# Optimization experiments

Measured on AMD Instinct MI355X. Metric: run time of the kernel, lower is better.

Reference implementation:

```python
import jax, jax.numpy as jnp
import numpy as np

HEADS = 8
DIM_HEAD = 64
QUERY_DIM = 512
CONTEXT_DIM = 768
INNER = HEADS * DIM_HEAD  # 512
SCALE = DIM_HEAD ** -0.5


def setup_inputs() -> dict:
    key = jax.random.key(0)
    ks = jax.random.split(key, 7)
    B, N, M = 4, 2048, 2048
    x = jax.random.normal(ks[0], (B, N, QUERY_DIM), dtype=jnp.float32)
    context = jax.random.normal(ks[1], (B, M, CONTEXT_DIM), dtype=jnp.float32)
    # torch Linear weights: [out_features, in_features], y = x @ W.T
    s = 0.02
    Wq = jax.random.normal(ks[2], (INNER, QUERY_DIM), dtype=jnp.float32) * s
    Wk = jax.random.normal(ks[3], (INNER, CONTEXT_DIM), dtype=jnp.float32) * s
    Wv = jax.random.normal(ks[4], (INNER, CONTEXT_DIM), dtype=jnp.float32) * s
    Wo = jax.random.normal(ks[5], (QUERY_DIM, INNER), dtype=jnp.float32) * s
    bo = jax.random.normal(ks[6], (QUERY_DIM,), dtype=jnp.float32) * s
    return {"x": x, "context": context, "Wq": Wq, "Wk": Wk, "Wv": Wv, "Wo": Wo, "bo": bo}


def reference(x, context, Wq, Wk, Wv, Wo, bo):
    b, n, _ = x.shape
    m = context.shape[1]
    h, d = HEADS, DIM_HEAD
    # Projections (bias=False for q/k/v)
    q = jnp.einsum('bnc,ec->bne', x, Wq)        # [b, n, inner]
    k = jnp.einsum('bmc,ec->bme', context, Wk)  # [b, m, inner]
    v = jnp.einsum('bmc,ec->bme', context, Wv)
    # Split heads
    q = q.reshape(b, n, h, d)
    k = k.reshape(b, m, h, d)
    v = v.reshape(b, m, h, d)
    # Scores in fp32 (original casts q,k to float), scaled by dim_head**-0.5
    sim = jnp.einsum('bihd,bjhd->bhij', q.astype(jnp.float32), k.astype(jnp.float32)) * SCALE
    attn = jax.nn.softmax(sim, axis=-1).astype(v.dtype)
    out = jnp.einsum('bhij,bjhd->bihd', attn, v).reshape(b, n, h * d)
    # Output projection with bias (dropout=0 -> identity)
    return jnp.einsum('bne,oe->bno', out, Wo) + bo
```

## Files before the change

### kernel.cpp

```cpp
#include <hip/hip_runtime.h>
#include <hip/hip_bf16.h>
#include <math.h>


typedef __bf16 bf16x8 __attribute__((ext_vector_type(8)));
typedef __bf16 bf16x4 __attribute__((ext_vector_type(4)));
typedef float f32x4 __attribute__((ext_vector_type(4)));

#define QSCALE 0.18033688011112042f

#if __has_builtin(__builtin_amdgcn_exp2f)
#define EXP2(x) __builtin_amdgcn_exp2f(x)
#else
#define EXP2(x) exp2f(x)
#endif

__device__ __forceinline__ f32x4 mfma32(bf16x8 a, bf16x8 b, f32x4 c) {
  return __builtin_amdgcn_mfma_f32_16x16x32_bf16(a, b, c, 0, 0, 0);
}

__device__ __forceinline__ void st_cast16(__bf16* dst, float4 f0, float4 f1,
                                          float4 f2, float4 f3) {
  union { __bf16 b[16]; uint4 u[2]; } cv;
  cv.b[0] = (__bf16)f0.x;  cv.b[1] = (__bf16)f0.y;
  cv.b[2] = (__bf16)f0.z;  cv.b[3] = (__bf16)f0.w;
  cv.b[4] = (__bf16)f1.x;  cv.b[5] = (__bf16)f1.y;
  cv.b[6] = (__bf16)f1.z;  cv.b[7] = (__bf16)f1.w;
  cv.b[8] = (__bf16)f2.x;  cv.b[9] = (__bf16)f2.y;
  cv.b[10] = (__bf16)f2.z; cv.b[11] = (__bf16)f2.w;
  cv.b[12] = (__bf16)f3.x; cv.b[13] = (__bf16)f3.y;
  cv.b[14] = (__bf16)f3.z; cv.b[15] = (__bf16)f3.w;
  ((uint4*)dst)[0] = cv.u[0];
  ((uint4*)dst)[1] = cv.u[1];
}

__global__ __launch_bounds__(256) void cast_w(
    const float* __restrict__ wq, const float* __restrict__ wk,
    const float* __restrict__ wv, const float* __restrict__ wo,
    __bf16* __restrict__ wqb, __bf16* __restrict__ wkb,
    __bf16* __restrict__ wvb, __bf16* __restrict__ wob) {
  const int B0 = 65536;
  const int B1 = 163840;
  const int B2 = 262144;
  const int B3 = 327680;
  for (int i = blockIdx.x * blockDim.x + threadIdx.x; i < B3;
       i += gridDim.x * blockDim.x) {
    const float* s;
    __bf16* d;
    int off;
    if (i < B0)      { s = wq; d = wqb; off = i; }
    else if (i < B1) { s = wk; d = wkb; off = i - B0; }
    else if (i < B2) { s = wv; d = wvb; off = i - B1; }
    else             { s = wo; d = wob; off = i - B2; }
    float4 f = ((const float4*)s)[off];
    union { __bf16 b[4]; ushort4 u; } cv;
    cv.b[0] = (__bf16)f.x; cv.b[1] = (__bf16)f.y;
    cv.b[2] = (__bf16)f.z; cv.b[3] = (__bf16)f.w;
    ((ushort4*)d)[off] = cv.u;
  }
}

template <int MODE>
__device__ __forceinline__ void gemm_body(
    const float* __restrict__ A, const __bf16* __restrict__ W,
    __bf16* __restrict__ Cout, int Kd, float scale, int m0, int n0,
    __bf16 (*As)[72], __bf16 (*Bs)[72]) {
  const int t = threadIdx.x;
  const int w = t >> 6;
  const int lane = t & 63;
  const int ln = lane & 15;
  const int qd = lane >> 4;
  const int wm = (w >> 1) * 64;
  const int wn = (w & 1) * 64;

  f32x4 zero4 = {0.f, 0.f, 0.f, 0.f};
  f32x4 acc[4][4];
#pragma unroll
  for (int i = 0; i < 4; ++i)
#pragma unroll
    for (int j = 0; j < 4; ++j) acc[i][j] = zero4;

  const int r0 = t >> 2;
  const int c0 = (t & 3) * 16;
  const float* gA0 = A + (size_t)(m0 + r0) * Kd + c0;
  const float* gA1 = A + (size_t)(m0 + r0 + 64) * Kd + c0;
  const __bf16* gB0 = W + (size_t)(n0 + r0) * Kd + c0;
  const __bf16* gB1 = W + (size_t)(n0 + r0 + 64) * Kd + c0;

  float4 a0[4], a1[4];
#pragma unroll
  for (int j = 0; j < 4; ++j) {
    a0[j] = ((const float4*)gA0)[j];
    a1[j] = ((const float4*)gA1)[j];
  }
  uint4 b00 = *(const uint4*)gB0, b01 = *(const uint4*)(gB0 + 8);
  uint4 b10 = *(const uint4*)gB1, b11 = *(const uint4*)(gB1 + 8);

  for (int kc = 0; kc < Kd; kc += 64) {
    __syncthreads();
    st_cast16(&As[r0][c0], a0[0], a0[1], a0[2], a0[3]);
    st_cast16(&As[r0 + 64][c0], a1[0], a1[1], a1[2], a1[3]);
    *(uint4*)&Bs[r0][c0] = b00;       *(uint4*)&Bs[r0][c0 + 8] = b01;
    *(uint4*)&Bs[r0 + 64][c0] = b10;  *(uint4*)&Bs[r0 + 64][c0 + 8] = b11;
    __syncthreads();
    if (kc + 64 < Kd) {
#pragma unroll
      for (int j = 0; j < 4; ++j) {
        a0[j] = ((const float4*)(gA0 + kc + 64))[j];
        a1[j] = ((const float4*)(gA1 + kc + 64))[j];
      }
      b00 = *(const uint4*)(gB0 + kc + 64);
      b01 = *(const uint4*)(gB0 + kc + 72);
      b10 = *(const uint4*)(gB1 + kc + 64);
      b11 = *(const uint4*)(gB1 + kc + 72);
    }
#pragma unroll
    for (int kst = 0; kst < 2; ++kst) {
      bf16x8 af[4], bfr[4];
#pragma unroll
      for (int i = 0; i < 4; ++i) {
        af[i] = *(const bf16x8*)&As[wm + i * 16 + ln][kst * 32 + qd * 8];
        bfr[i] = *(const bf16x8*)&Bs[wn + i * 16 + ln][kst * 32 + qd * 8];
      }
#pragma unroll
      for (int i = 0; i < 4; ++i)
#pragma unroll
        for (int j = 0; j < 4; ++j) {
          if (MODE == 1)
            acc[i][j] = mfma32(af[i], bfr[j], acc[i][j]);
          else
            acc[i][j] = mfma32(bfr[j], af[i], acc[i][j]);
        }
    }
  }

#pragma unroll
  for (int i = 0; i < 4; ++i)
#pragma unroll
    for (int j = 0; j < 4; ++j) {
      if (MODE == 0) {
        const int gm = m0 + wm + i * 16 + ln;
        const int gn0 = n0 + wn + j * 16 + qd * 4;
        const int bb = gm >> 11, tok = gm & 2047;
        const int hh = gn0 >> 6, dd0 = gn0 & 63;
        bf16x4 v;
#pragma unroll
        for (int rg = 0; rg < 4; ++rg) v[rg] = (__bf16)(acc[i][j][rg] * scale);
        *(bf16x4*)(Cout + (((size_t)bb * 8 + hh) * 2048 + tok) * 64 + dd0) = v;
      } else {
        const int gm0 = m0 + wm + i * 16 + qd * 4;
        const int gn = n0 + wn + j * 16 + ln;
        const int bb = gm0 >> 11, tok0 = gm0 & 2047;
        const int hh = gn >> 6, dd = gn & 63;
        bf16x4 v;
#pragma unroll
        for (int rg = 0; rg < 4; ++rg) v[rg] = (__bf16)acc[i][j][rg];
        *(bf16x4*)(Cout + (((size_t)bb * 8 + hh) * 64 + dd) * 2048 + tok0) = v;
      }
    }
}

__global__ __launch_bounds__(256, 3) void proj_qkv(
    const float* __restrict__ x, const float* __restrict__ ctx,
    const __bf16* __restrict__ Wq, const __bf16* __restrict__ Wk,
    const __bf16* __restrict__ Wv, __bf16* __restrict__ Qw,
    __bf16* __restrict__ Kw, __bf16* __restrict__ Vtw) {
  __shared__ __align__(16) __bf16 As[128][72];
  __shared__ __align__(16) __bf16 Bs[128][72];
  const int m0 = blockIdx.x * 128;
  const int job = blockIdx.y >> 2;
  const int n0 = (blockIdx.y & 3) * 128;
  if (job == 0)
    gemm_body<0>(x, Wq, Qw, 512, QSCALE, m0, n0, As, Bs);
  else if (job == 1)
    gemm_body<0>(ctx, Wk, Kw, 768, 1.0f, m0, n0, As, Bs);
  else
    gemm_body<1>(ctx, Wv, Vtw, 768, 1.0f, m0, n0, As, Bs);
}

__global__ __launch_bounds__(256) void gemm_out(
    const __bf16* __restrict__ O0, const __bf16* __restrict__ O1,
    const float* __restrict__ lbuf,
    const __bf16* __restrict__ B,
    float* __restrict__ C, const float* __restrict__ bias) {
  const int m0 = blockIdx.x * 64;
  const int n0 = blockIdx.y * 128;
  const int t = threadIdx.x;
  const int w = t >> 6;
  const int lane = t & 63;
  const int ln = lane & 15;
  const int qd = lane >> 4;
  const int wm = (w >> 1) * 32;
  const int wn = (w & 1) * 64;

  __shared__ __align__(16) __bf16 As[64][72];
  __shared__ __align__(16) __bf16 Bs[128][72];

  f32x4 zero4 = {0.f, 0.f, 0.f, 0.f};
  f32x4 acc[2][4];
#pragma unroll
  for (int i = 0; i < 2; ++i)
#pragma unroll
    for (int j = 0; j < 4; ++j) acc[i][j] = zero4;

  const int r0 = t >> 2;
  const int c0 = (t & 3) * 16;
  const int gm_s = m0 + r0;
  const int bidx = gm_s >> 11, tok_s = gm_s & 2047;
  const size_t aoff = (size_t)gm_s * 512 + c0;
  const __bf16* gB0 = B + (size_t)(n0 + r0) * 512 + c0;
  const __bf16* gB1 = B + (size_t)(n0 + r0 + 64) * 512 + c0;

  float inv[8];
#pragma unroll
  for (int hh = 0; hh < 8; ++hh) {
    const float l0 = lbuf[((size_t)bidx * 8 + hh) * 2048 + tok_s];
    const float l1 = lbuf[65536 + ((size_t)bidx * 8 + hh) * 2048 + tok_s];
    inv[hh] = 1.0f / (l0 + l1);
  }

  uint4 o00 = *(const uint4*)(O0 + aoff), o01 = *(const uint4*)(O0 + aoff + 8);
  uint4 o10 = *(const uint4*)(O1 + aoff), o11 = *(const uint4*)(O1 + aoff + 8);
  uint4 b00 = *(const uint4*)gB0, b01 = *(const uint4*)(gB0 + 8);
  uint4 b10 = *(const uint4*)gB1, b11 = *(const uint4*)(gB1 + 8);

  for (int kc = 0; kc < 512; kc += 64) {
    const float iv = inv[kc >> 6];
    union { bf16x8 v; uint4 u; } u0, u1, r0v, r1v;
    u0.u = o00; u1.u = o10;
#pragma unroll
    for (int e = 0; e < 8; ++e)
      r0v.v[e] = (__bf16)(((float)u0.v[e] + (float)u1.v[e]) * iv);
    u0.u = o01; u1.u = o11;
#pragma unroll
    for (int e = 0; e < 8; ++e)
      r1v.v[e] = (__bf16)(((float)u0.v[e] + (float)u1.v[e]) * iv);
    __syncthreads();
    *(uint4*)&As[r0][c0] = r0v.u;
    *(uint4*)&As[r0][c0 + 8] = r1v.u;
    *(uint4*)&Bs[r0][c0] = b00;       *(uint4*)&Bs[r0][c0 + 8] = b01;
    *(uint4*)&Bs[r0 + 64][c0] = b10;  *(uint4*)&Bs[r0 + 64][c0 + 8] = b11;
    __syncthreads();
    if (kc + 64 < 512) {
      o00 = *(const uint4*)(O0 + aoff + kc + 64);
      o01 = *(const uint4*)(O0 + aoff + kc + 72);
      o10 = *(const uint4*)(O1 + aoff + kc + 64);
      o11 = *(const uint4*)(O1 + aoff + kc + 72);
      b00 = *(const uint4*)(gB0 + kc + 64);
      b01 = *(const uint4*)(gB0 + kc + 72);
      b10 = *(const uint4*)(gB1 + kc + 64);
      b11 = *(const uint4*)(gB1 + kc + 72);
    }
#pragma unroll
    for (int kst = 0; kst < 2; ++kst) {
      bf16x8 af[2], bfr[4];
#pragma unroll
      for (int i = 0; i < 2; ++i)
        af[i] = *(const bf16x8*)&As[wm + i * 16 + ln][kst * 32 + qd * 8];
#pragma unroll
      for (int j = 0; j < 4; ++j)
        bfr[j] = *(const bf16x8*)&Bs[wn + j * 16 + ln][kst * 32 + qd * 8];
#pragma unroll
      for (int i = 0; i < 2; ++i)
#pragma unroll
        for (int j = 0; j < 4; ++j)
          acc[i][j] = mfma32(bfr[j], af[i], acc[i][j]);
    }
  }

#pragma unroll
  for (int i = 0; i < 2; ++i)
#pragma unroll
    for (int j = 0; j < 4; ++j) {
      const int gm = m0 + wm + i * 16 + ln;
      const int gn0 = n0 + wn + j * 16 + qd * 4;
      f32x4 bi = *(const f32x4*)&bias[gn0];
      f32x4 v = acc[i][j] + bi;
      *(f32x4*)&C[(size_t)gm * 512 + gn0] = v;
    }
}

__global__ __launch_bounds__(256, 2) void attn_kernel(
    const __bf16* __restrict__ Q,
    const __bf16* __restrict__ K,
    const __bf16* __restrict__ Vt,
    __bf16* __restrict__ Oh,
    float* __restrict__ lbuf) {
  const int S = 2048;
  const int qt = blockIdx.x;
  const int bh = blockIdx.y;
  const int sp = blockIdx.z;
  const int b = bh >> 3, h = bh & 7;
  const int t = threadIdx.x;
  const int w = t >> 6;
  const int lane = t & 63;
  const int ln = lane & 15;
  const int qd = lane >> 4;

  __shared__ __align__(16) __bf16 Ks[2][128][72];
  __shared__ __align__(16) __bf16 Vs[2][64][136];

  bf16x8 bq[4][2];
  {
    const __bf16* qb =
        Q + ((size_t)bh * S + qt * 256 + w * 64 + ln) * 64 + qd * 8;
#pragma unroll
    for (int mt = 0; mt < 4; ++mt)
#pragma unroll
      for (int kst = 0; kst < 2; ++kst)
        bq[mt][kst] = *(const bf16x8*)(qb + mt * 1024 + kst * 32);
  }

  f32x4 zero4 = {0.f, 0.f, 0.f, 0.f};
  f32x4 o[4][4];
  f32x4 o_l[4];
#pragma unroll
  for (int mt = 0; mt < 4; ++mt) {
#pragma unroll
    for (int i = 0; i < 4; ++i) o[mt][i] = zero4;
    o_l[mt] = zero4;
  }
  bf16x8 ones8;
  {
    union { unsigned short u[8]; bf16x8 v; } U;
#pragma unroll
    for (int e = 0; e < 8; ++e) U.u[e] = 0x3F80;
    ones8 = U.v;
  }

  const int kr = t >> 2, kc0 = (t & 3) * 16;
  const int krow =
      (kr & ~31) | ((kr & 4) << 2) | (((kr >> 3) & 3) << 2) | (kr & 3);
  const int vd = t >> 3, vtok0 = (t & 7) * 16;
  const int kt0 = sp * 8;

  const __bf16* gK0 = K + ((size_t)bh * S + kt0 * 128 + kr) * 64 + kc0;
  const __bf16* gK1 = gK0 + 4096;
  const __bf16* gV0 = Vt + ((size_t)bh * 64 + vd) * S + kt0 * 128 + vtok0;
  const __bf16* gV1 = gV0 + 65536;

  {
    uint4 k00 = ((const uint4*)gK0)[0], k01 = ((const uint4*)gK0)[1];
    uint4 k10 = ((const uint4*)gK1)[0], k11 = ((const uint4*)gK1)[1];
    uint4 v00 = ((const uint4*)gV0)[0], v01 = ((const uint4*)gV0)[1];
    uint4 v10 = ((const uint4*)gV1)[0], v11 = ((const uint4*)gV1)[1];
    uint4* dK0 = (uint4*)&Ks[0][krow][kc0];      dK0[0] = k00; dK0[1] = k01;
    uint4* dK1 = (uint4*)&Ks[0][krow + 64][kc0]; dK1[0] = k10; dK1[1] = k11;
    uint4* dV0 = (uint4*)&Vs[0][vd][vtok0];      dV0[0] = v00; dV0[1] = v01;
    uint4* dV1 = (uint4*)&Vs[0][vd + 32][vtok0]; dV1[0] = v10; dV1[1] = v11;
  }
  uint4 pk00 = ((const uint4*)(gK0 + 8192))[0];
  uint4 pk01 = ((const uint4*)(gK0 + 8192))[1];
  uint4 pk10 = ((const uint4*)(gK1 + 8192))[0];
  uint4 pk11 = ((const uint4*)(gK1 + 8192))[1];
  uint4 pv00 = ((const uint4*)(gV0 + 128))[0];
  uint4 pv01 = ((const uint4*)(gV0 + 128))[1];
  uint4 pv10 = ((const uint4*)(gV1 + 128))[0];
  uint4 pv11 = ((const uint4*)(gV1 + 128))[1];
  __syncthreads();

  int p = 0;
  for (int it = 0; it < 8; ++it) {
    if (it + 1 < 8) {
      uint4* dK0 = (uint4*)&Ks[p ^ 1][krow][kc0];
      dK0[0] = pk00; dK0[1] = pk01;
      uint4* dK1 = (uint4*)&Ks[p ^ 1][krow + 64][kc0];
      dK1[0] = pk10; dK1[1] = pk11;
      uint4* dV0 = (uint4*)&Vs[p ^ 1][vd][vtok0];
      dV0[0] = pv00; dV0[1] = pv01;
      uint4* dV1 = (uint4*)&Vs[p ^ 1][vd + 32][vtok0];
      dV1[0] = pv10; dV1[1] = pv11;
      if (it + 2 < 8) {
        const __bf16* nK0 = gK0 + (size_t)(it + 2) * 8192;
        const __bf16* nK1 = gK1 + (size_t)(it + 2) * 8192;
        const __bf16* nV0 = gV0 + (size_t)(it + 2) * 128;
        const __bf16* nV1 = gV1 + (size_t)(it + 2) * 128;
        pk00 = ((const uint4*)nK0)[0]; pk01 = ((const uint4*)nK0)[1];
        pk10 = ((const uint4*)nK1)[0]; pk11 = ((const uint4*)nK1)[1];
        pv00 = ((const uint4*)nV0)[0]; pv01 = ((const uint4*)nV0)[1];
        pv10 = ((const uint4*)nV1)[0]; pv11 = ((const uint4*)nV1)[1];
      }
    }

    const __bf16 (*Ksp)[72] = Ks[p];
    const __bf16 (*Vsp)[136] = Vs[p];

#pragma unroll
    for (int c = 0; c < 4; ++c) {
      bf16x8 ak[2][2];
#pragma unroll
      for (int e = 0; e < 2; ++e)
#pragma unroll
        for (int kst = 0; kst < 2; ++kst)
          ak[e][kst] =
              *(const bf16x8*)&Ksp[(c * 2 + e) * 16 + ln][kst * 32 + qd * 8];
      bf16x8 av[4];
#pragma unroll
      for (int i = 0; i < 4; ++i)
        av[i] = *(const bf16x8*)&Vsp[i * 16 + ln][c * 32 + qd * 8];

#pragma unroll
      for (int mt = 0; mt < 4; ++mt) {
        f32x4 s0 = zero4, s1 = zero4;
        __builtin_amdgcn_s_setprio(1);
#pragma unroll
        for (int kst = 0; kst < 2; ++kst) {
          s0 = mfma32(ak[0][kst], bq[mt][kst], s0);
          s1 = mfma32(ak[1][kst], bq[mt][kst], s1);
        }
        __builtin_amdgcn_s_setprio(0);
#pragma unroll
        for (int rg = 0; rg < 4; ++rg) {
          s0[rg] = EXP2(s0[rg]);
          s1[rg] = EXP2(s1[rg]);
        }
        bf16x8 p2;
#pragma unroll
        for (int rg = 0; rg < 4; ++rg) {
          p2[rg] = (__bf16)s0[rg];
          p2[rg + 4] = (__bf16)s1[rg];
        }
        __builtin_amdgcn_s_setprio(1);
        o_l[mt] = mfma32(ones8, p2, o_l[mt]);
#pragma unroll
        for (int i = 0; i < 4; ++i)
          o[mt][i] = mfma32(av[i], p2, o[mt][i]);
        __builtin_amdgcn_s_setprio(0);
      }
    }

    __syncthreads();
    p ^= 1;
  }

  __bf16* Osp = Oh + (size_t)sp * 8192 * 512;
#pragma unroll
  for (int mt = 0; mt < 4; ++mt) {
    const int tok = qt * 256 + w * 64 + mt * 16 + ln;
    if (qd == 0) lbuf[((size_t)sp * 32 + bh) * 2048 + tok] = o_l[mt][0];
#pragma unroll
    for (int i = 0; i < 4; ++i) {
      bf16x4 v;
#pragma unroll
      for (int rg = 0; rg < 4; ++rg) v[rg] = (__bf16)o[mt][i][rg];
      const int col = h * 64 + i * 16 + qd * 4;
      *(bf16x4*)&Osp[((size_t)b * S + tok) * 512 + col] = v;
    }
  }
}

extern "C" void kernel_launch(void* const* d_in, const int* in_sizes, int n_in,
                              void* d_out, int out_size, void* d_ws,
                              size_t ws_size, hipStream_t stream) {
  const float* x = (const float*)d_in[0];
  const float* ctx = (const float*)d_in[1];
  const float* Wq = (const float*)d_in[2];
  const float* Wk = (const float*)d_in[3];
  const float* Wv = (const float*)d_in[4];
  const float* Wo = (const float*)d_in[5];
  const float* bo = (const float*)d_in[6];

  char* p = (char*)d_ws;
  __bf16* wqb = (__bf16*)p;  p += (size_t)512 * 512 * 2;
  __bf16* wkb = (__bf16*)p;  p += (size_t)512 * 768 * 2;
  __bf16* wvb = (__bf16*)p;  p += (size_t)512 * 768 * 2;
  __bf16* wob = (__bf16*)p;  p += (size_t)512 * 512 * 2;
  __bf16* Qw = (__bf16*)p;   p += (size_t)8192 * 512 * 2;
  __bf16* Kw = (__bf16*)p;   p += (size_t)8192 * 512 * 2;
  __bf16* Vtw = (__bf16*)p;  p += (size_t)8192 * 512 * 2;
  __bf16* Oh = (__bf16*)p;   p += (size_t)2 * 8192 * 512 * 2;
  float* lbuf = (float*)p;   p += (size_t)2 * 32 * 2048 * 4;

  cast_w<<<1280, 256, 0, stream>>>(Wq, Wk, Wv, Wo, wqb, wkb, wvb, wob);

  dim3 gp(64, 12);
  proj_qkv<<<gp, 256, 0, stream>>>(x, ctx, wqb, wkb, wvb, Qw, Kw, Vtw);

  dim3 ga(8, 32, 2);
  attn_kernel<<<ga, 256, 0, stream>>>(Qw, Kw, Vtw, Oh, lbuf);

  dim3 go(128, 4);
  gemm_out<<<go, 256, 0, stream>>>(Oh, Oh + (size_t)8192 * 512, lbuf, wob,
                                   (float*)d_out, bo);
}
```

Measured before the change: 178.9 us.

## Switch attention inner loop to 32x32x16 MFMA and compute row sums on VALU

```diff
diff --git a/kernel.cpp b/kernel.cpp
--- a/kernel.cpp
+++ b/kernel.cpp
@@ -6,6 +6,7 @@
 typedef __bf16 bf16x8 __attribute__((ext_vector_type(8)));
 typedef __bf16 bf16x4 __attribute__((ext_vector_type(4)));
 typedef float f32x4 __attribute__((ext_vector_type(4)));
+typedef float f32x16 __attribute__((ext_vector_type(16)));
 
 #define QSCALE 0.18033688011112042f
 
@@ -17,6 +18,10 @@
 
 __device__ __forceinline__ f32x4 mfma32(bf16x8 a, bf16x8 b, f32x4 c) {
   return __builtin_amdgcn_mfma_f32_16x16x32_bf16(a, b, c, 0, 0, 0);
+}
+
+__device__ __forceinline__ f32x16 mfma3216(bf16x8 a, bf16x8 b, f32x16 c) {
+  return __builtin_amdgcn_mfma_f32_32x32x16_bf16(a, b, c, 0, 0, 0);
 }
 
 __device__ __forceinline__ void st_cast16(__bf16* dst, float4 f0, float4 f1,
@@ -294,43 +299,35 @@
   const int t = threadIdx.x;
   const int w = t >> 6;
   const int lane = t & 63;
-  const int ln = lane & 15;
-  const int qd = lane >> 4;
+  const int ln5 = lane & 31;
+  const int hi = lane >> 5;
 
   __shared__ __align__(16) __bf16 Ks[2][128][72];
   __shared__ __align__(16) __bf16 Vs[2][64][136];
 
-  bf16x8 bq[4][2];
+  const int qbase = qt * 256 + w * 64;
+
+  bf16x8 bq[2][4];
   {
-    const __bf16* qb =
-        Q + ((size_t)bh * S + qt * 256 + w * 64 + ln) * 64 + qd * 8;
-#pragma unroll
-    for (int mt = 0; mt < 4; ++mt)
-#pragma unroll
-      for (int kst = 0; kst < 2; ++kst)
-        bq[mt][kst] = *(const bf16x8*)(qb + mt * 1024 + kst * 32);
-  }
-
-  f32x4 zero4 = {0.f, 0.f, 0.f, 0.f};
-  f32x4 o[4][4];
-  f32x4 o_l[4];
-#pragma unroll
-  for (int mt = 0; mt < 4; ++mt) {
-#pragma unroll
-    for (int i = 0; i < 4; ++i) o[mt][i] = zero4;
-    o_l[mt] = zero4;
-  }
-  bf16x8 ones8;
-  {
-    union { unsigned short u[8]; bf16x8 v; } U;
-#pragma unroll
-    for (int e = 0; e < 8; ++e) U.u[e] = 0x3F80;
-    ones8 = U.v;
-  }
+    const __bf16* qb = Q + ((size_t)bh * S + qbase + ln5) * 64 + hi * 8;
+#pragma unroll
+    for (int mt = 0; mt < 2; ++mt)
+#pragma unroll
+      for (int ks = 0; ks < 4; ++ks)
+        bq[mt][ks] = *(const bf16x8*)(qb + mt * 32 * 64 + ks * 16);
+  }
+
+  f32x16 zero16 = {0.f, 0.f, 0.f, 0.f, 0.f, 0.f, 0.f, 0.f,
+                   0.f, 0.f, 0.f, 0.f, 0.f, 0.f, 0.f, 0.f};
+  f32x16 oacc[2][2];
+#pragma unroll
+  for (int mt = 0; mt < 2; ++mt)
+#pragma unroll
+    for (int dh = 0; dh < 2; ++dh) oacc[mt][dh] = zero16;
+  float l_acc[2] = {0.f, 0.f};
 
   const int kr = t >> 2, kc0 = (t & 3) * 16;
-  const int krow =
-      (kr & ~31) | ((kr & 4) << 2) | (((kr >> 3) & 3) << 2) | (kr & 3);
+  const int krow = (kr & ~12) | ((kr & 4) << 1) | ((kr & 8) >> 1);
   const int vd = t >> 3, vtok0 = (t & 7) * 16;
   const int kt0 = sp * 8;
 
@@ -386,45 +383,44 @@
     const __bf16 (*Vsp)[136] = Vs[p];
 
 #pragma unroll
-    for (int c = 0; c < 4; ++c) {
-      bf16x8 ak[2][2];
-#pragma unroll
-      for (int e = 0; e < 2; ++e)
-#pragma unroll
-        for (int kst = 0; kst < 2; ++kst)
-          ak[e][kst] =
-              *(const bf16x8*)&Ksp[(c * 2 + e) * 16 + ln][kst * 32 + qd * 8];
-      bf16x8 av[4];
-#pragma unroll
-      for (int i = 0; i < 4; ++i)
-        av[i] = *(const bf16x8*)&Vsp[i * 16 + ln][c * 32 + qd * 8];
-
-#pragma unroll
-      for (int mt = 0; mt < 4; ++mt) {
-        f32x4 s0 = zero4, s1 = zero4;
+    for (int g = 0; g < 4; ++g) {
+      bf16x8 kf[4];
+#pragma unroll
+      for (int ks = 0; ks < 4; ++ks)
+        kf[ks] = *(const bf16x8*)&Ksp[g * 32 + ln5][ks * 16 + hi * 8];
+      bf16x8 vf[2][2];
+#pragma unroll
+      for (int sub = 0; sub < 2; ++sub)
+#pragma unroll
+        for (int dh = 0; dh < 2; ++dh)
+          vf[sub][dh] = *(const bf16x8*)
+              &Vsp[dh * 32 + ln5][g * 32 + sub * 16 + hi * 8];
+
+#pragma unroll
+      for (int mt = 0; mt < 2; ++mt) {
+        f32x16 s = zero16;
         __builtin_amdgcn_s_setprio(1);
 #pragma unroll
-        for (int kst = 0; kst < 2; ++kst) {
-          s0 = mfma32(ak[0][kst], bq[mt][kst], s0);
-          s1 = mfma32(ak[1][kst], bq[mt][kst], s1);
+        for (int ks = 0; ks < 4; ++ks) s = mfma3216(kf[ks], bq[mt][ks], s);
+        __builtin_amdgcn_s_setprio(0);
+        float la = 0.f;
+#pragma unroll
+        for (int r = 0; r < 16; ++r) {
+          s[r] = EXP2(s[r]);
+          la += s[r];
         }
-        __builtin_amdgcn_s_setprio(0);
-#pragma unroll
-        for (int rg = 0; rg < 4; ++rg) {
-          s0[rg] = EXP2(s0[rg]);
-          s1[rg] = EXP2(s1[rg]);
-        }
-        bf16x8 p2;
-#pragma unroll
-        for (int rg = 0; rg < 4; ++rg) {
-          p2[rg] = (__bf16)s0[rg];
-          p2[rg + 4] = (__bf16)s1[rg];
+        l_acc[mt] += la;
+        bf16x8 p0, p1;
+#pragma unroll
+        for (int j = 0; j < 8; ++j) {
+          p0[j] = (__bf16)s[j];
+          p1[j] = (__bf16)s[j + 8];
         }
         __builtin_amdgcn_s_setprio(1);
-        o_l[mt] = mfma32(ones8, p2, o_l[mt]);
-#pragma unroll
-        for (int i = 0; i < 4; ++i)
-          o[mt][i] = mfma32(av[i], p2, o[mt][i]);
+        oacc[mt][0] = mfma3216(vf[0][0], p0, oacc[mt][0]);
+        oacc[mt][1] = mfma3216(vf[0][1], p0, oacc[mt][1]);
+        oacc[mt][0] = mfma3216(vf[1][0], p1, oacc[mt][0]);
+        oacc[mt][1] = mfma3216(vf[1][1], p1, oacc[mt][1]);
         __builtin_amdgcn_s_setprio(0);
       }
     }
@@ -435,17 +431,20 @@
 
   __bf16* Osp = Oh + (size_t)sp * 8192 * 512;
 #pragma unroll
-  for (int mt = 0; mt < 4; ++mt) {
-    const int tok = qt * 256 + w * 64 + mt * 16 + ln;
-    if (qd == 0) lbuf[((size_t)sp * 32 + bh) * 2048 + tok] = o_l[mt][0];
-#pragma unroll
-    for (int i = 0; i < 4; ++i) {
-      bf16x4 v;
-#pragma unroll
-      for (int rg = 0; rg < 4; ++rg) v[rg] = (__bf16)o[mt][i][rg];
-      const int col = h * 64 + i * 16 + qd * 4;
-      *(bf16x4*)&Osp[((size_t)b * S + tok) * 512 + col] = v;
-    }
+  for (int mt = 0; mt < 2; ++mt) {
+    float l = l_acc[mt] + __shfl_xor(l_acc[mt], 32, 64);
+    const int tok = qbase + mt * 32 + ln5;
+    if (hi == 0) lbuf[((size_t)sp * 32 + bh) * 2048 + tok] = l;
+#pragma unroll
+    for (int dh = 0; dh < 2; ++dh)
+#pragma unroll
+      for (int rgg = 0; rgg < 4; ++rgg) {
+        bf16x4 v;
+#pragma unroll
+        for (int e = 0; e < 4; ++e) v[e] = (__bf16)oacc[mt][dh][rgg * 4 + e];
+        const int d0 = dh * 32 + 4 * hi + 8 * rgg;
+        *(bf16x4*)&Osp[((size_t)b * S + tok) * 512 + h * 64 + d0] = v;
+      }
   }
 }
 
```

Measured after the change: 180.4 us. No clear change (+0.8%).
